# Performance work log

Hardware: AMD Instinct MI355X
Metric: run time of the kernel (lower is better)

Reference implementation:

```python
import jax, jax.numpy as jnp
import numpy as np

N = 100000      # nodes
E = 1600000     # edges
G = 64          # graphs in batch
H = 128         # hidden (== num_features)
L = 4           # num_layers
C = 16          # num_classes
NCAND = 100000  # candidate edges
BN_EPS = 1e-5


def setup_inputs() -> dict:
    key = jax.random.key(0)
    ks = jax.random.split(key, 24)
    s = 0.05
    inp = {}
    inp["x"] = jax.random.normal(ks[0], (N, H), dtype=jnp.float32)
    inp["edge_index"] = jax.random.randint(ks[1], (2, E), 0, N)
    inp["batch"] = jnp.sort(jax.random.randint(ks[2], (N,), 0, G))
    inp["candidate_edges"] = jax.random.randint(ks[3], (2, NCAND), 0, N)
    # GIN conv params, stacked over L layers (all layers are H->H since num_features==hidden)
    inp["cW1"] = jax.random.normal(ks[4], (L, H, H), dtype=jnp.float32) * s
    inp["cb1"] = jnp.zeros((L, H), jnp.float32)
    inp["cW2"] = jax.random.normal(ks[5], (L, H, H), dtype=jnp.float32) * s
    inp["cb2"] = jnp.zeros((L, H), jnp.float32)
    inp["cgamma"] = jnp.ones((L, H), jnp.float32)
    inp["cbeta"] = jnp.zeros((L, H), jnp.float32)
    inp["ceps"] = jnp.zeros((L,), jnp.float32)  # train_eps=True, init 0
    # node classifier: L*H -> 2H -> H -> H -> C (dropout is identity in eval)
    inp["ncW1"] = jax.random.normal(ks[6], (L * H, 2 * H), dtype=jnp.float32) * s
    inp["ncb1"] = jnp.zeros((2 * H,), jnp.float32)
    inp["ncW2"] = jax.random.normal(ks[7], (2 * H, H), dtype=jnp.float32) * s
    inp["ncb2"] = jnp.zeros((H,), jnp.float32)
    inp["ncW3"] = jax.random.normal(ks[8], (H, H), dtype=jnp.float32) * s
    inp["ncb3"] = jnp.zeros((H,), jnp.float32)
    inp["ncW4"] = jax.random.normal(ks[9], (H, C), dtype=jnp.float32) * s
    inp["ncb4"] = jnp.zeros((C,), jnp.float32)
    # edge predictor: 2*L*H -> 2H -> H -> 1
    inp["epW1"] = jax.random.normal(ks[10], (2 * L * H, 2 * H), dtype=jnp.float32) * s
    inp["epb1"] = jnp.zeros((2 * H,), jnp.float32)
    inp["epW2"] = jax.random.normal(ks[11], (2 * H, H), dtype=jnp.float32) * s
    inp["epb2"] = jnp.zeros((H,), jnp.float32)
    inp["epW3"] = jax.random.normal(ks[12], (H, 1), dtype=jnp.float32) * s
    inp["epb3"] = jnp.zeros((1,), jnp.float32)
    return inp


def _forward(x, cW1, cb1, cW2, cb2, cgamma, cbeta, ceps,
             ncW1, ncb1, ncW2, ncb2, ncW3, ncb3, ncW4, ncb4,
             epW1, epb1, epW2, epb2, epW3, epb3,
             edge_index, batch, candidate_edges):
    src, dst = edge_index[0], edge_index[1]
    h = x
    xs = []
    for l in range(L):
        # GIN: (1+eps)*x_i + sum_{j->i} x_j  (scatter-add over destination nodes)
        agg = jax.ops.segment_sum(h[src], dst, num_segments=N)
        z = (1.0 + ceps[l]) * h + agg
        z = jax.nn.relu(z @ cW1[l] + cb1[l])
        z = jax.nn.relu(z @ cW2[l] + cb2[l])
        # BatchNorm1d (training-mode batch statistics, biased variance)
        mu = z.mean(axis=0)
        var = jnp.var(z, axis=0)
        h = (z - mu) * jax.lax.rsqrt(var + BN_EPS) * cgamma[l] + cbeta[l]
        xs.append(h)
    emb = jnp.concatenate(xs, axis=-1)  # [N, L*H]
    # global mean pool over graphs
    sums = jax.ops.segment_sum(emb, batch, num_segments=G)
    cnt = jax.ops.segment_sum(jnp.ones((N, 1), emb.dtype), batch, num_segments=G)
    gemb = sums / jnp.maximum(cnt, 1.0)  # [G, L*H]
    t = jax.nn.relu(gemb @ ncW1 + ncb1)
    t = jax.nn.relu(t @ ncW2 + ncb2)
    t = jax.nn.relu(t @ ncW3 + ncb3)
    class_output = jax.nn.log_softmax(t @ ncW4 + ncb4, axis=1)  # [G, C]
    # link prediction: gather node embeddings per candidate edge
    ef = jnp.concatenate([emb[candidate_edges[0]], emb[candidate_edges[1]]], axis=1)  # [NC, 2*L*H]
    u = jax.nn.relu(ef @ epW1 + epb1)
    u = jax.nn.relu(u @ epW2 + epb2)
    edge_scores = jax.nn.sigmoid((u @ epW3 + epb3).squeeze(-1))  # [NC]
    return class_output, edge_scores


def reference(x, cW1, cb1, cW2, cb2, cgamma, cbeta, ceps,
              ncW1, ncb1, ncW2, ncb2, ncW3, ncb3, ncW4, ncb4,
              epW1, epb1, epW2, epb2, epW3, epb3,
              edge_index, batch, candidate_edges):
    return _forward(x, cW1, cb1, cW2, cb2, cgamma, cbeta, ceps,
                    ncW1, ncb1, ncW2, ncb2, ncW3, ncb3, ncW4, ncb4,
                    epW1, epb1, epW2, epb2, epW3, epb3,
                    edge_index, batch, candidate_edges)
```

## Files before the change

kernel.cpp:

```cpp
#include <hip/hip_runtime.h>
#include <math.h>

#define NN 100000
#define EE 1600000
#define GG 64
#define HH 128
#define LL 4
#define CCLS 16
#define NC 100000
#define NB 49
#define LDK 40
#define LDA2 136

typedef __attribute__((ext_vector_type(8))) short bf16x8;
typedef __attribute__((ext_vector_type(4))) float f32x4;

__device__ __forceinline__ unsigned short f2bf(float x) {
  union { float f; unsigned int u; } v; v.f = x;
  unsigned int r = v.u + 0x7fffu + ((v.u >> 16) & 1u);
  return (unsigned short)(r >> 16);
}
__device__ __forceinline__ float bl(unsigned u) {
  union { unsigned u; float f; } v; v.u = u << 16; return v.f;
}
__device__ __forceinline__ float bh(unsigned u) {
  union { unsigned u; float f; } v; v.u = u & 0xffff0000u; return v.f;
}

__global__ void hist_kernel(const int* __restrict__ dst, int* __restrict__ cnt, int E) {
  int e = blockIdx.x * 256 + threadIdx.x;
  if (e < E) atomicAdd(&cnt[dst[e]], 1);
}

__global__ __launch_bounds__(256) void scan_p1(const int* __restrict__ cnt,
                                               int* __restrict__ bsum, int n) {
  __shared__ int red[256];
  int tid = threadIdx.x;
  int base = blockIdx.x * 1024 + tid * 4;
  int s = 0;
  if (base + 3 < n) {
    int4 v = *(const int4*)(cnt + base);
    s = v.x + v.y + v.z + v.w;
  } else {
    for (int i = 0; i < 4; ++i) if (base + i < n) s += cnt[base + i];
  }
  red[tid] = s;
  __syncthreads();
  for (int st = 128; st >= 1; st >>= 1) {
    if (tid < st) red[tid] += red[tid + st];
    __syncthreads();
  }
  if (tid == 0) bsum[blockIdx.x] = red[0];
}

__global__ void scan_p2(int* __restrict__ bsum, int* __restrict__ rowptr,
                        int* __restrict__ bcursor, int nb, int n) {
  __shared__ int buf[128];
  int tid = threadIdx.x;
  int v = (tid < nb) ? bsum[tid] : 0;
  buf[tid] = v;
  __syncthreads();
  for (int off = 1; off < 128; off <<= 1) {
    int t = (tid >= off) ? buf[tid - off] : 0;
    __syncthreads();
    buf[tid] += t;
    __syncthreads();
  }
  if (tid < nb) bsum[tid] = buf[tid] - v;
  if (tid == 127) rowptr[n] = buf[127];
  __syncthreads();
  if (tid < NB) bcursor[tid] = bsum[2 * tid];
}

__global__ __launch_bounds__(256) void scan_p3(const int* __restrict__ cnt,
                                               const int* __restrict__ bsum,
                                               int* __restrict__ rowptr,
                                               int* __restrict__ cursor, int n) {
  __shared__ int red[256];
  int tid = threadIdx.x;
  int base = blockIdx.x * 1024 + tid * 4;
  int v[4] = {0, 0, 0, 0};
  if (base + 3 < n) {
    int4 t = *(const int4*)(cnt + base);
    v[0] = t.x; v[1] = t.y; v[2] = t.z; v[3] = t.w;
  } else {
    for (int i = 0; i < 4; ++i) if (base + i < n) v[i] = cnt[base + i];
  }
  int s = v[0] + v[1] + v[2] + v[3];
  red[tid] = s;
  __syncthreads();
  for (int off = 1; off < 256; off <<= 1) {
    int t = (tid >= off) ? red[tid - off] : 0;
    __syncthreads();
    red[tid] += t;
    __syncthreads();
  }
  int run = bsum[blockIdx.x] + red[tid] - s;
  int4 o;
  o.x = run; o.y = run + v[0]; o.z = o.y + v[1]; o.w = o.z + v[2];
  if (base + 3 < n) {
    *(int4*)(rowptr + base) = o;
    *(int4*)(cursor + base) = o;
  } else {
    int oo[4] = {o.x, o.y, o.z, o.w};
    for (int i = 0; i < 4; ++i)
      if (base + i < n) { rowptr[base + i] = oo[i]; cursor[base + i] = oo[i]; }
  }
}

__global__ __launch_bounds__(256) void partition_kernel(const int* __restrict__ src,
                                                        const int* __restrict__ dst,
                                                        int* __restrict__ bcursor,
                                                        int2* __restrict__ pairs, int E) {
  __shared__ int sS[4096];
  __shared__ int sD[4096];
  __shared__ int hist[NB];
  __shared__ int base[NB];
  int tid = threadIdx.x;
  int base_e = blockIdx.x * 4096;
  int cnt = min(4096, E - base_e);
  if (tid < NB) hist[tid] = 0;
  for (int i = tid * 4; i < cnt; i += 1024) {
    if (i + 3 < cnt) {
      *(int4*)(sS + i) = *(const int4*)(src + base_e + i);
      *(int4*)(sD + i) = *(const int4*)(dst + base_e + i);
    } else {
      for (int k = i; k < cnt; ++k) { sS[k] = src[base_e + k]; sD[k] = dst[base_e + k]; }
    }
  }
  __syncthreads();
  for (int i = tid; i < cnt; i += 256) atomicAdd(&hist[sD[i] >> 11], 1);
  __syncthreads();
  if (tid < NB) {
    base[tid] = atomicAdd(&bcursor[tid], hist[tid]);
    hist[tid] = 0;
  }
  __syncthreads();
  for (int i = tid; i < cnt; i += 256) {
    int d = sD[i];
    int b = d >> 11;
    int off = atomicAdd(&hist[b], 1);
    pairs[base[b] + off] = make_int2(sS[i], d);
  }
}

__global__ __launch_bounds__(256) void scatter_csr(const int2* __restrict__ pairs,
                                                   const int* __restrict__ rowptr,
                                                   int* __restrict__ cursor,
                                                   int* __restrict__ csr_src) {
  int b = blockIdx.x % 56;
  int slice = blockIdx.x / 56;
  if (b >= NB) return;
  int start = rowptr[b * 2048];
  int endn = min((b + 1) * 2048, NN);
  int end = rowptr[endn];
  for (int i = start + slice * 256 + threadIdx.x; i < end; i += 8 * 256) {
    int2 p = pairs[i];
    int pos = atomicAdd(&cursor[p.y], 1);
    csr_src[pos] = p.x;
  }
}

__global__ void f2b4_kernel(const float* __restrict__ in, unsigned short* __restrict__ out, int n4) {
  int i = blockIdx.x * 256 + threadIdx.x;
  if (i >= n4) return;
  float4 v = ((const float4*)in)[i];
  unsigned short r[4] = {f2bf(v.x), f2bf(v.y), f2bf(v.z), f2bf(v.w)};
  *(uint2*)(out + (size_t)i * 4) = *(uint2*)r;
}

__global__ void conv_weights(const float* __restrict__ cW1, const float* __restrict__ cW2,
                             unsigned short* __restrict__ WT1, unsigned short* __restrict__ WT2,
                             const float* __restrict__ epW1, unsigned short* __restrict__ W1T,
                             const float* __restrict__ epW2, unsigned short* __restrict__ W2T) {
  int idx = blockIdx.x * 256 + threadIdx.x;
  if (idx < LL * 16384) {
    int l = idx >> 14, r = idx & 16383, k = r >> 7, n = r & 127;
    WT1[l * 16384 + n * 128 + k] = f2bf(cW1[idx]);
    WT2[l * 16384 + n * 128 + k] = f2bf(cW2[idx]);
  } else if (idx < LL * 16384 + 262144) {
    int j = idx - LL * 16384;
    int k = j >> 8, n = j & 255;
    W1T[(size_t)n * 1024 + k] = f2bf(epW1[j]);
  } else if (idx < LL * 16384 + 262144 + 32768) {
    int j = idx - LL * 16384 - 262144;
    int k = j >> 7, n = j & 127;
    W2T[(size_t)n * 256 + k] = f2bf(epW2[j]);
  }
}

__global__ void aggregate_bf16(const unsigned short* __restrict__ h16, int ld,
                               const int* __restrict__ rowptr,
                               const int* __restrict__ csr_src,
                               const float* __restrict__ ceps_l,
                               unsigned short* __restrict__ out, int n) {
  int wave = threadIdx.x >> 6;
  int lane = threadIdx.x & 63;
  int sub = lane >> 4;
  int li = lane & 15;
  int node = blockIdx.x * 16 + wave * 4 + sub;
  if (node >= n) return;
  int c8 = li * 8;
  float eps1 = 1.0f + *ceps_l;
  float acc[8] = {};
  int b = rowptr[node], e = rowptr[node + 1];
  int j = b;
  for (; j + 8 <= e; j += 8) {
    uint4 u[8];
#pragma unroll
    for (int t = 0; t < 8; ++t) {
      int s = csr_src[j + t];
      u[t] = *(const uint4*)(h16 + (size_t)s * ld + c8);
    }
#pragma unroll
    for (int t = 0; t < 8; ++t) {
      acc[0] += bl(u[t].x); acc[1] += bh(u[t].x);
      acc[2] += bl(u[t].y); acc[3] += bh(u[t].y);
      acc[4] += bl(u[t].z); acc[5] += bh(u[t].z);
      acc[6] += bl(u[t].w); acc[7] += bh(u[t].w);
    }
  }
  for (; j < e; ++j) {
    int s = csr_src[j];
    uint4 u = *(const uint4*)(h16 + (size_t)s * ld + c8);
    acc[0] += bl(u.x); acc[1] += bh(u.x);
    acc[2] += bl(u.y); acc[3] += bh(u.y);
    acc[4] += bl(u.z); acc[5] += bh(u.z);
    acc[6] += bl(u.w); acc[7] += bh(u.w);
  }
  uint4 hu = *(const uint4*)(h16 + (size_t)node * ld + c8);
  acc[0] = fmaf(eps1, bl(hu.x), acc[0]); acc[1] = fmaf(eps1, bh(hu.x), acc[1]);
  acc[2] = fmaf(eps1, bl(hu.y), acc[2]); acc[3] = fmaf(eps1, bh(hu.y), acc[3]);
  acc[4] = fmaf(eps1, bl(hu.z), acc[4]); acc[5] = fmaf(eps1, bh(hu.z), acc[5]);
  acc[6] = fmaf(eps1, bl(hu.w), acc[6]); acc[7] = fmaf(eps1, bh(hu.w), acc[7]);
  unsigned short o[8];
#pragma unroll
  for (int i = 0; i < 8; ++i) o[i] = f2bf(acc[i]);
  *(uint4*)(out + (size_t)node * 128 + c8) = *(uint4*)o;
}

__global__ __launch_bounds__(256) void trunk_fused(
    const unsigned short* __restrict__ A16,
    const unsigned short* __restrict__ W1T, const float* __restrict__ b1,
    const unsigned short* __restrict__ W2T, const float* __restrict__ b2,
    float* __restrict__ bnsum, float* __restrict__ bnsumsq,
    unsigned short* __restrict__ C16, int M) {
  __shared__ unsigned short As[128 * LDA2];
  __shared__ unsigned short Bs[128 * LDK];
  const int tid = threadIdx.x;
  const int bm = blockIdx.x * 128;
  const int lane = tid & 63;
  const int wave = tid >> 6;
  const int wr = (wave >> 1) << 6;
  const int wc = (wave & 1) << 6;
  const int ar = tid >> 1;
  const int ah = (tid & 1) << 4;
  int gra = bm + ar; if (gra >= M) gra = M - 1;
  const unsigned short* Arow = A16 + (size_t)gra * 128;
  const int mrow = lane & 15;
  const int kq = (lane >> 4) << 3;
  f32x4 acc[4][4] = {};

#pragma unroll
  for (int ks = 0; ks < 4; ++ks) {
    const int k0 = ks << 5;
    const uint4* s = (const uint4*)(Arow + k0 + ah);
    *(uint4*)(As + ar * LDA2 + k0 + ah) = s[0];
    *(uint4*)(As + ar * LDA2 + k0 + ah + 8) = s[1];
  }
  uint4 p0 = *(const uint4*)(W1T + (size_t)ar * 128 + ah);
  uint4 p1 = *(const uint4*)(W1T + (size_t)ar * 128 + ah + 8);
  for (int ks = 0; ks < 4; ++ks) {
    const int k0 = ks << 5;
    *(uint4*)(Bs + ar * LDK + ah) = p0;
    *(uint4*)(Bs + ar * LDK + ah + 8) = p1;
    __syncthreads();
    if (ks < 3) {
      p0 = *(const uint4*)(W1T + (size_t)ar * 128 + k0 + 32 + ah);
      p1 = *(const uint4*)(W1T + (size_t)ar * 128 + k0 + 32 + ah + 8);
    }
    bf16x8 af[4], bfv[4];
#pragma unroll
    for (int t = 0; t < 4; ++t)
      af[t] = *(const bf16x8*)(As + (wr + t * 16 + mrow) * LDA2 + k0 + kq);
#pragma unroll
    for (int t = 0; t < 4; ++t)
      bfv[t] = *(const bf16x8*)(Bs + (wc + t * 16 + mrow) * LDK + kq);
#pragma unroll
    for (int mt = 0; mt < 4; ++mt)
#pragma unroll
      for (int nt = 0; nt < 4; ++nt)
        acc[mt][nt] = __builtin_amdgcn_mfma_f32_16x16x32_bf16(af[mt], bfv[nt], acc[mt][nt], 0, 0, 0);
    __syncthreads();
  }
  const int crow = (lane >> 4) << 2;
  const int ccol = lane & 15;
#pragma unroll
  for (int nt = 0; nt < 4; ++nt) {
    int c = wc + nt * 16 + ccol;
    float bz = b1[c];
#pragma unroll
    for (int mt = 0; mt < 4; ++mt) {
      int rl = wr + mt * 16 + crow;
#pragma unroll
      for (int i = 0; i < 4; ++i)
        As[(rl + i) * LDA2 + c] = f2bf(fmaxf(acc[mt][nt][i] + bz, 0.f));
    }
  }
#pragma unroll
  for (int mt = 0; mt < 4; ++mt)
#pragma unroll
    for (int nt = 0; nt < 4; ++nt)
      acc[mt][nt] = (f32x4){0.f, 0.f, 0.f, 0.f};
  p0 = *(const uint4*)(W2T + (size_t)ar * 128 + ah);
  p1 = *(const uint4*)(W2T + (size_t)ar * 128 + ah + 8);
  __syncthreads();
  for (int ks = 0; ks < 4; ++ks) {
    const int k0 = ks << 5;
    *(uint4*)(Bs + ar * LDK + ah) = p0;
    *(uint4*)(Bs + ar * LDK + ah + 8) = p1;
    __syncthreads();
    if (ks < 3) {
      p0 = *(const uint4*)(W2T + (size_t)ar * 128 + k0 + 32 + ah);
      p1 = *(const uint4*)(W2T + (size_t)ar * 128 + k0 + 32 + ah + 8);
    }
    bf16x8 af[4], bfv[4];
#pragma unroll
    for (int t = 0; t < 4; ++t)
      af[t] = *(const bf16x8*)(As + (wr + t * 16 + mrow) * LDA2 + k0 + kq);
#pragma unroll
    for (int t = 0; t < 4; ++t)
      bfv[t] = *(const bf16x8*)(Bs + (wc + t * 16 + mrow) * LDK + kq);
#pragma unroll
    for (int mt = 0; mt < 4; ++mt)
#pragma unroll
      for (int nt = 0; nt < 4; ++nt)
        acc[mt][nt] = __builtin_amdgcn_mfma_f32_16x16x32_bf16(af[mt], bfv[nt], acc[mt][nt], 0, 0, 0);
    __syncthreads();
  }
#pragma unroll
  for (int nt = 0; nt < 4; ++nt) {
    int c = wc + nt * 16 + ccol;
    float bz = b2[c];
    float s = 0.f, q = 0.f;
#pragma unroll
    for (int mt = 0; mt < 4; ++mt) {
      int rbase = bm + wr + mt * 16 + crow;
#pragma unroll
      for (int i = 0; i < 4; ++i) {
        int r = rbase + i;
        if (r < M) {
          float v = fmaxf(acc[mt][nt][i] + bz, 0.f);
          C16[(size_t)r * 128 + c] = f2bf(v);
          s += v; q += v * v;
        }
      }
    }
    s += __shfl_xor(s, 16, 64);
    s += __shfl_xor(s, 32, 64);
    q += __shfl_xor(q, 16, 64);
    q += __shfl_xor(q, 32, 64);
    if (lane < 16) {
      atomicAdd(&bnsum[c], s);
      atomicAdd(&bnsumsq[c], q);
    }
  }
}

__global__ __launch_bounds__(512) void mfma_gemm_gather(
    const unsigned short* __restrict__ emb16, const int* __restrict__ cand,
    const unsigned short* __restrict__ WT ,
    const float* __restrict__ bias,
    unsigned short* __restrict__ C16 , int M) {
  __shared__ unsigned short As[2][128 * LDK];
  __shared__ unsigned short Bs[2][256 * LDK];
  const int tid = threadIdx.x;
  const int bm = blockIdx.x * 128;
  const int lane = tid & 63;
  const int wave = tid >> 6;
  const int wr = (wave >> 2) << 6;
  const int wc = (wave & 3) << 6;
  f32x4 acc[4][4] = {};
  const int ar = tid >> 2;
  const int ah = (tid & 3) << 3;
  int gra = bm + ar; if (gra >= M) gra = M - 1;
  const int node0 = cand[gra];
  const int node1 = cand[NC + gra];
  const int br = tid >> 1;
  const int bh8 = (tid & 1) << 4;
  const unsigned short* Brow = WT + (size_t)br * 1024 + bh8;
  const int mrow = lane & 15;
  const int kq = (lane >> 4) << 3;

  {
    uint4 a = *(const uint4*)(emb16 + (size_t)node0 * 512 + ah);
    uint4 b0 = *(const uint4*)(Brow);
    uint4 b1 = *(const uint4*)(Brow + 8);
    *(uint4*)(As[0] + ar * LDK + ah) = a;
    *(uint4*)(Bs[0] + br * LDK + bh8) = b0;
    *(uint4*)(Bs[0] + br * LDK + bh8 + 8) = b1;
  }
  __syncthreads();
  for (int ks = 0; ks < 32; ++ks) {
    const int cur = ks & 1, nxt = cur ^ 1;
    uint4 a, b0, b1;
    if (ks < 31) {
      const int k1 = (ks + 1) << 5;
      int node = (k1 < 512) ? node0 : node1;
      a = *(const uint4*)(emb16 + (size_t)node * 512 + (k1 & 511) + ah);
      b0 = *(const uint4*)(Brow + k1);
      b1 = *(const uint4*)(Brow + k1 + 8);
    }
    bf16x8 af[4], bfv[4];
#pragma unroll
    for (int t = 0; t < 4; ++t)
      af[t] = *(const bf16x8*)(As[cur] + (wr + t * 16 + mrow) * LDK + kq);
#pragma unroll
    for (int t = 0; t < 4; ++t)
      bfv[t] = *(const bf16x8*)(Bs[cur] + (wc + t * 16 + mrow) * LDK + kq);
#pragma unroll
    for (int mt = 0; mt < 4; ++mt)
#pragma unroll
      for (int nt = 0; nt < 4; ++nt)
        acc[mt][nt] = __builtin_amdgcn_mfma_f32_16x16x32_bf16(af[mt], bfv[nt], acc[mt][nt], 0, 0, 0);
    if (ks < 31) {
      *(uint4*)(As[nxt] + ar * LDK + ah) = a;
      *(uint4*)(Bs[nxt] + br * LDK + bh8) = b0;
      *(uint4*)(Bs[nxt] + br * LDK + bh8 + 8) = b1;
      __syncthreads();
    }
  }
  const int crow = (lane >> 4) << 2;
  const int ccol = lane & 15;
#pragma unroll
  for (int nt = 0; nt < 4; ++nt) {
    int cbase = wc + nt * 16 + ccol;
    float bz = bias[cbase];
#pragma unroll
    for (int mt = 0; mt < 4; ++mt) {
      int rbase = bm + wr + mt * 16 + crow;
#pragma unroll
      for (int i = 0; i < 4; ++i) {
        int r = rbase + i;
        if (r < M) C16[(size_t)r * 256 + cbase] = f2bf(fmaxf(acc[mt][nt][i] + bz, 0.f));
      }
    }
  }
}

__global__ __launch_bounds__(256) void ep_gemm2_final(
    const unsigned short* __restrict__ A16 ,
    const unsigned short* __restrict__ WT ,
    const float* __restrict__ b2, const float* __restrict__ epW3,
    const float* __restrict__ epb3,
    float* __restrict__ out, int M) {
  __shared__ unsigned short As[2][128 * LDK];
  __shared__ unsigned short Bs[2][128 * LDK];
  __shared__ float sDot[128];
  const int tid = threadIdx.x;
  const int bm = blockIdx.x * 128;
  const int lane = tid & 63;
  const int wave = tid >> 6;
  const int wr = (wave >> 1) << 6;
  const int wc = (wave & 1) << 6;
  f32x4 acc[4][4] = {};
  const int ar = tid >> 1;
  const int ah = (tid & 1) << 4;
  int gra = bm + ar; if (gra >= M) gra = M - 1;
  const unsigned short* Arow = A16 + (size_t)gra * 256;
  const unsigned short* Brow = WT + (size_t)ar * 256;
  const int mrow = lane & 15;
  const int kq = (lane >> 4) << 3;

  if (tid < 128) sDot[tid] = 0.f;
  {
    uint4 a0 = *(const uint4*)(Arow + ah);
    uint4 a1 = *(const uint4*)(Arow + ah + 8);
    uint4 b0 = *(const uint4*)(Brow + ah);
    uint4 b1 = *(const uint4*)(Brow + ah + 8);
    *(uint4*)(As[0] + ar * LDK + ah) = a0;
    *(uint4*)(As[0] + ar * LDK + ah + 8) = a1;
    *(uint4*)(Bs[0] + ar * LDK + ah) = b0;
    *(uint4*)(Bs[0] + ar * LDK + ah + 8) = b1;
  }
  __syncthreads();
  for (int ks = 0; ks < 8; ++ks) {
    const int cur = ks & 1, nxt = cur ^ 1;
    uint4 a0, a1, b0, b1;
    if (ks < 7) {
      const int k1 = (ks + 1) << 5;
      a0 = *(const uint4*)(Arow + k1 + ah);
      a1 = *(const uint4*)(Arow + k1 + ah + 8);
      b0 = *(const uint4*)(Brow + k1 + ah);
      b1 = *(const uint4*)(Brow + k1 + ah + 8);
    }
    bf16x8 af[4], bfv[4];
#pragma unroll
    for (int t = 0; t < 4; ++t)
      af[t] = *(const bf16x8*)(As[cur] + (wr + t * 16 + mrow) * LDK + kq);
#pragma unroll
    for (int t = 0; t < 4; ++t)
      bfv[t] = *(const bf16x8*)(Bs[cur] + (wc + t * 16 + mrow) * LDK + kq);
#pragma unroll
    for (int mt = 0; mt < 4; ++mt)
#pragma unroll
      for (int nt = 0; nt < 4; ++nt)
        acc[mt][nt] = __builtin_amdgcn_mfma_f32_16x16x32_bf16(af[mt], bfv[nt], acc[mt][nt], 0, 0, 0);
    if (ks < 7) {
      *(uint4*)(As[nxt] + ar * LDK + ah) = a0;
      *(uint4*)(As[nxt] + ar * LDK + ah + 8) = a1;
      *(uint4*)(Bs[nxt] + ar * LDK + ah) = b0;
      *(uint4*)(Bs[nxt] + ar * LDK + ah + 8) = b1;
      __syncthreads();
    }
  }
  const int crow = (lane >> 4) << 2;
  const int ccol = lane & 15;
  float w3v[4], bz[4];
#pragma unroll
  for (int nt = 0; nt < 4; ++nt) {
    int c = wc + nt * 16 + ccol;
    w3v[nt] = epW3[c];
    bz[nt] = b2[c];
  }
  __syncthreads();
#pragma unroll
  for (int mt = 0; mt < 4; ++mt) {
#pragma unroll
    for (int i = 0; i < 4; ++i) {
      int rl = wr + mt * 16 + crow + i;
      float p = 0.f;
#pragma unroll
      for (int nt = 0; nt < 4; ++nt)
        p = fmaf(fmaxf(acc[mt][nt][i] + bz[nt], 0.f), w3v[nt], p);
      atomicAdd(&sDot[rl], p);
    }
  }
  __syncthreads();
  if (tid < 128) {
    int r = bm + tid;
    if (r < M) out[r] = 1.f / (1.f + expf(-(sDot[tid] + epb3[0])));
  }
}

__global__ void bn_apply_bf16(const unsigned short* __restrict__ z,
                              const float* __restrict__ sum, const float* __restrict__ sumsq,
                              const float* __restrict__ gamma, const float* __restrict__ beta,
                              unsigned short* __restrict__ out, int n) {
  int idx = blockIdx.x * 256 + threadIdx.x;
  if (idx >= n * 16) return;
  int r = idx >> 4, c8 = (idx & 15) << 3;
  uint4 v = *(const uint4*)(z + (size_t)r * 128 + c8);
  float f[8] = {bl(v.x), bh(v.x), bl(v.y), bh(v.y), bl(v.z), bh(v.z), bl(v.w), bh(v.w)};
  const float inv_n = 1.0f / (float)NN;
  unsigned short o[8];
#pragma unroll
  for (int j = 0; j < 8; ++j) {
    int c = c8 + j;
    float mu = sum[c] * inv_n;
    float var = sumsq[c] * inv_n - mu * mu;
    float sc = rsqrtf(var + 1e-5f) * gamma[c];
    o[j] = f2bf((f[j] - mu) * sc + beta[c]);
  }
  *(uint4*)(out + (size_t)r * 512 + c8) = *(uint4*)o;
}

__global__ void bounds_kernel(const int* __restrict__ batch, int* __restrict__ gstart, int n) {
  int g = threadIdx.x;
  if (g > GG) return;
  int lo = 0, hi = n;
  while (lo < hi) {
    int mid = (lo + hi) >> 1;
    if (batch[mid] < g) lo = mid + 1; else hi = mid;
  }
  gstart[g] = lo;
}

__global__ __launch_bounds__(256) void pool_bf16(const unsigned short* __restrict__ emb16,
                                                 const int* __restrict__ gstart,
                                                 float* __restrict__ gsum) {
  int g = blockIdx.x;
  int chunk = blockIdx.y;
  int c2 = threadIdx.x * 2;
  int s = gstart[g], e = gstart[g + 1];
  int len = e - s;
  int per = (len + 7) >> 3;
  int r0 = s + chunk * per;
  int r1 = min(r0 + per, e);
  float ax = 0.f, ay = 0.f;
  for (int r = r0; r < r1; ++r) {
    unsigned u = *(const unsigned*)(emb16 + (size_t)r * 512 + c2);
    ax += bl(u); ay += bh(u);
  }
  if (r1 > r0) {
    atomicAdd(&gsum[g * 512 + c2], ax);
    atomicAdd(&gsum[g * 512 + c2 + 1], ay);
  }
}

__global__ __launch_bounds__(256) void nc_fused(
    const float* __restrict__ gsum, const int* __restrict__ gstart,
    const float* __restrict__ W1, const float* __restrict__ b1,
    const float* __restrict__ W2, const float* __restrict__ b2,
    const float* __restrict__ W3, const float* __restrict__ b3,
    const float* __restrict__ W4, const float* __restrict__ b4,
    float* __restrict__ out) {
  __shared__ float row[512];
  __shared__ float t1[256];
  __shared__ float t2[128];
  __shared__ float t3s[128];
  __shared__ float lg[16];
  int g = blockIdx.x;
  int tid = threadIdx.x;
  float inv = 1.0f / fmaxf((float)(gstart[g + 1] - gstart[g]), 1.0f);
  row[tid] = gsum[g * 512 + tid] * inv;
  row[tid + 256] = gsum[g * 512 + tid + 256] * inv;
  __syncthreads();
  {
    float acc = b1[tid];
#pragma unroll 8
    for (int k = 0; k < 512; ++k) acc = fmaf(row[k], W1[k * 256 + tid], acc);
    t1[tid] = fmaxf(acc, 0.f);
  }
  __syncthreads();
  if (tid < 128) {
    float acc = b2[tid];
#pragma unroll 8
    for (int k = 0; k < 256; ++k) acc = fmaf(t1[k], W2[k * 128 + tid], acc);
    t2[tid] = fmaxf(acc, 0.f);
  }
  __syncthreads();
  if (tid < 128) {
    float acc = b3[tid];
#pragma unroll 8
    for (int k = 0; k < 128; ++k) acc = fmaf(t2[k], W3[k * 128 + tid], acc);
    t3s[tid] = fmaxf(acc, 0.f);
  }
  __syncthreads();
  if (tid < 16) {
    float acc = b4[tid];
#pragma unroll 8
    for (int k = 0; k < 128; ++k) acc = fmaf(t3s[k], W4[k * 16 + tid], acc);
    lg[tid] = acc;
  }
  __syncthreads();
  if (tid < 16) {
    float v = lg[tid];
    float m = v;
    for (int j = 0; j < 16; ++j) m = fmaxf(m, lg[j]);
    float s = 0.f;
    for (int j = 0; j < 16; ++j) s += expf(lg[j] - m);
    out[g * 16 + tid] = v - m - logf(s);
  }
}

extern "C" void kernel_launch(void* const* d_in, const int* in_sizes, int n_in,
                              void* d_out, int out_size, void* d_ws, size_t ws_size,
                              hipStream_t stream) {
  const float* x = (const float*)d_in[0];
  const int* edge_index = (const int*)d_in[1];
  const int* batch = (const int*)d_in[2];
  const int* cand = (const int*)d_in[3];
  const float* cW1 = (const float*)d_in[4];
  const float* cb1 = (const float*)d_in[5];
  const float* cW2 = (const float*)d_in[6];
  const float* cb2 = (const float*)d_in[7];
  const float* cgamma = (const float*)d_in[8];
  const float* cbeta = (const float*)d_in[9];
  const float* ceps = (const float*)d_in[10];
  const float* ncW1 = (const float*)d_in[11];
  const float* ncb1 = (const float*)d_in[12];
  const float* ncW2 = (const float*)d_in[13];
  const float* ncb2 = (const float*)d_in[14];
  const float* ncW3 = (const float*)d_in[15];
  const float* ncb3 = (const float*)d_in[16];
  const float* ncW4 = (const float*)d_in[17];
  const float* ncb4 = (const float*)d_in[18];
  const float* epW1 = (const float*)d_in[19];
  const float* epb1 = (const float*)d_in[20];
  const float* epW2 = (const float*)d_in[21];
  const float* epb2 = (const float*)d_in[22];
  const float* epW3 = (const float*)d_in[23];
  const float* epb3 = (const float*)d_in[24];

  char* ws = (char*)d_ws;
  size_t off = 0;
  auto alloc = [&](size_t bytes) -> void* {
    off = (off + 255) & ~(size_t)255;
    void* p = ws + off;
    off += bytes;
    return p;
  };
  size_t zz_bytes = (size_t)NN * 4 + 512 * 4 + 512 * 4 + (size_t)GG * 512 * 4;
  char* zz = (char*)alloc(zz_bytes);
  int* cnt = (int*)zz;
  float* bnsum = (float*)(zz + (size_t)NN * 4);
  float* bnsumsq = bnsum + 512;
  float* gsum = bnsumsq + 512;
  int* rowptr = (int*)alloc((size_t)(NN + 1) * 4);
  int* cursor = (int*)alloc((size_t)NN * 4);
  int* csr_src = (int*)alloc((size_t)EE * 4);
  int2* pairs = (int2*)alloc((size_t)EE * 8);
  int* bsum = (int*)alloc(128 * 4);
  int* bcursor = (int*)alloc(64 * 4);
  unsigned short* x16 = (unsigned short*)alloc((size_t)NN * 128 * 2);
  unsigned short* g16a = (unsigned short*)alloc((size_t)NN * 128 * 2);
  unsigned short* emb16 = (unsigned short*)alloc((size_t)NN * 512 * 2);
  unsigned short* C1 = (unsigned short*)alloc((size_t)NC * 256 * 2);
  unsigned short* WT1 = (unsigned short*)alloc((size_t)LL * 16384 * 2);
  unsigned short* WT2 = (unsigned short*)alloc((size_t)LL * 16384 * 2);
  unsigned short* W1T = (unsigned short*)alloc((size_t)1024 * 256 * 2);
  unsigned short* W2T = (unsigned short*)alloc((size_t)256 * 128 * 2);
  int* gstart = (int*)alloc(65 * 4);

  const int* esrc = edge_index;
  const int* edst = edge_index + EE;
  const int nblk = (NN + 1023) / 1024;
  const int nech = (EE + 4095) / 4096;

  hipMemsetAsync(zz, 0, zz_bytes, stream);
  hist_kernel<<<(EE + 255) / 256, 256, 0, stream>>>(edst, cnt, EE);
  scan_p1<<<nblk, 256, 0, stream>>>(cnt, bsum, NN);
  scan_p2<<<1, 128, 0, stream>>>(bsum, rowptr, bcursor, nblk, NN);
  scan_p3<<<nblk, 256, 0, stream>>>(cnt, bsum, rowptr, cursor, NN);
  partition_kernel<<<nech, 256, 0, stream>>>(esrc, edst, bcursor, pairs, EE);
  scatter_csr<<<56 * 8, 256, 0, stream>>>(pairs, rowptr, cursor, csr_src);
  f2b4_kernel<<<(NN * 128 / 4 + 255) / 256, 256, 0, stream>>>(x, x16, NN * 128 / 4);
  conv_weights<<<(LL * 16384 + 262144 + 32768 + 255) / 256, 256, 0, stream>>>(
      cW1, cW2, WT1, WT2, epW1, W1T, epW2, W2T);

  for (int l = 0; l < LL; ++l) {
    const unsigned short* h16 = (l == 0) ? x16 : (emb16 + (size_t)(l - 1) * 128);
    int ld = (l == 0) ? 128 : 512;
    aggregate_bf16<<<(NN + 15) / 16, 256, 0, stream>>>(h16, ld, rowptr, csr_src, ceps + l, g16a, NN);
    trunk_fused<<<(NN + 127) / 128, 256, 0, stream>>>(
        g16a, WT1 + (size_t)l * 16384, cb1 + l * 128,
        WT2 + (size_t)l * 16384, cb2 + l * 128,
        bnsum + l * 128, bnsumsq + l * 128, g16a, NN);
    bn_apply_bf16<<<(NN * 16 + 255) / 256, 256, 0, stream>>>(
        g16a, bnsum + l * 128, bnsumsq + l * 128, cgamma + l * 128, cbeta + l * 128,
        emb16 + (size_t)l * 128, NN);
  }

  bounds_kernel<<<1, 128, 0, stream>>>(batch, gstart, NN);
  pool_bf16<<<dim3(GG, 8), 256, 0, stream>>>(emb16, gstart, gsum);
  nc_fused<<<GG, 256, 0, stream>>>(gsum, gstart, ncW1, ncb1, ncW2, ncb2, ncW3, ncb3,
                                   ncW4, ncb4, (float*)d_out);

  mfma_gemm_gather<<<(NC + 127) / 128, 512, 0, stream>>>(emb16, cand, W1T, epb1, C1, NC);
  ep_gemm2_final<<<(NC + 127) / 128, 256, 0, stream>>>(C1, W2T, epb2, epW3, epb3,
                                                       (float*)d_out + GG * CCLS, NC);
}
```

Before: 1.120 ms.

## Fuse aggregation into layer GEMM and fold BatchNorm into downstream consumers

The separate per-layer aggregation and BN-apply kernels are removed. Each layer kernel now gathers neighbour rows straight into shared memory, applies the previous layer's BN affine analytically (scaling the sum and adding degree times the shift), then runs the MLP and writes raw post-ReLU activations into the embedding buffer. The final BN affine is folded into the edge-predictor first-layer weights and bias and into the pooled graph embeddings. This removes several full-size bf16 round trips and launches per layer. The cost is gather work serialized within each GEMM block, which may hurt latency hiding, and some extra rounding from the folded weights.

New measurement: 1.231 ms. 9.9% more time.

```diff
diff --git a/kernel.cpp b/kernel.cpp
--- a/kernel.cpp
+++ b/kernel.cpp
@@ -171,80 +171,59 @@
 
 __global__ void conv_weights(const float* __restrict__ cW1, const float* __restrict__ cW2,
                              unsigned short* __restrict__ WT1, unsigned short* __restrict__ WT2,
-                             const float* __restrict__ epW1, unsigned short* __restrict__ W1T,
                              const float* __restrict__ epW2, unsigned short* __restrict__ W2T) {
   int idx = blockIdx.x * 256 + threadIdx.x;
   if (idx < LL * 16384) {
     int l = idx >> 14, r = idx & 16383, k = r >> 7, n = r & 127;
     WT1[l * 16384 + n * 128 + k] = f2bf(cW1[idx]);
     WT2[l * 16384 + n * 128 + k] = f2bf(cW2[idx]);
-  } else if (idx < LL * 16384 + 262144) {
+  } else if (idx < LL * 16384 + 32768) {
     int j = idx - LL * 16384;
-    int k = j >> 8, n = j & 255;
-    W1T[(size_t)n * 1024 + k] = f2bf(epW1[j]);
-  } else if (idx < LL * 16384 + 262144 + 32768) {
-    int j = idx - LL * 16384 - 262144;
     int k = j >> 7, n = j & 127;
     W2T[(size_t)n * 256 + k] = f2bf(epW2[j]);
   }
 }
 
-__global__ void aggregate_bf16(const unsigned short* __restrict__ h16, int ld,
-                               const int* __restrict__ rowptr,
-                               const int* __restrict__ csr_src,
-                               const float* __restrict__ ceps_l,
-                               unsigned short* __restrict__ out, int n) {
-  int wave = threadIdx.x >> 6;
-  int lane = threadIdx.x & 63;
-  int sub = lane >> 4;
-  int li = lane & 15;
-  int node = blockIdx.x * 16 + wave * 4 + sub;
-  if (node >= n) return;
-  int c8 = li * 8;
-  float eps1 = 1.0f + *ceps_l;
-  float acc[8] = {};
-  int b = rowptr[node], e = rowptr[node + 1];
-  int j = b;
-  for (; j + 8 <= e; j += 8) {
-    uint4 u[8];
-#pragma unroll
-    for (int t = 0; t < 8; ++t) {
-      int s = csr_src[j + t];
-      u[t] = *(const uint4*)(h16 + (size_t)s * ld + c8);
-    }
-#pragma unroll
-    for (int t = 0; t < 8; ++t) {
-      acc[0] += bl(u[t].x); acc[1] += bh(u[t].x);
-      acc[2] += bl(u[t].y); acc[3] += bh(u[t].y);
-      acc[4] += bl(u[t].z); acc[5] += bh(u[t].z);
-      acc[6] += bl(u[t].w); acc[7] += bh(u[t].w);
-    }
-  }
-  for (; j < e; ++j) {
-    int s = csr_src[j];
-    uint4 u = *(const uint4*)(h16 + (size_t)s * ld + c8);
-    acc[0] += bl(u.x); acc[1] += bh(u.x);
-    acc[2] += bl(u.y); acc[3] += bh(u.y);
-    acc[4] += bl(u.z); acc[5] += bh(u.z);
-    acc[6] += bl(u.w); acc[7] += bh(u.w);
-  }
-  uint4 hu = *(const uint4*)(h16 + (size_t)node * ld + c8);
-  acc[0] = fmaf(eps1, bl(hu.x), acc[0]); acc[1] = fmaf(eps1, bh(hu.x), acc[1]);
-  acc[2] = fmaf(eps1, bl(hu.y), acc[2]); acc[3] = fmaf(eps1, bh(hu.y), acc[3]);
-  acc[4] = fmaf(eps1, bl(hu.z), acc[4]); acc[5] = fmaf(eps1, bh(hu.z), acc[5]);
-  acc[6] = fmaf(eps1, bl(hu.w), acc[6]); acc[7] = fmaf(eps1, bh(hu.w), acc[7]);
-  unsigned short o[8];
-#pragma unroll
-  for (int i = 0; i < 8; ++i) o[i] = f2bf(acc[i]);
-  *(uint4*)(out + (size_t)node * 128 + c8) = *(uint4*)o;
-}
-
-__global__ __launch_bounds__(256) void trunk_fused(
-    const unsigned short* __restrict__ A16,
+__global__ void bn_coef(const float* __restrict__ bnsum, const float* __restrict__ bnsumsq,
+                        const float* __restrict__ cgamma, const float* __restrict__ cbeta,
+                        float* __restrict__ abuf, float* __restrict__ bbuf) {
+  int c = blockIdx.x * 256 + threadIdx.x;
+  if (c >= 512) return;
+  const float inv_n = 1.0f / (float)NN;
+  float mu = bnsum[c] * inv_n;
+  float var = bnsumsq[c] * inv_n - mu * mu;
+  float sc = rsqrtf(var + 1e-5f) * cgamma[c];
+  abuf[c] = sc;
+  bbuf[c] = cbeta[c] - mu * sc;
+}
+
+__global__ void fold_w1(const float* __restrict__ epW1, const float* __restrict__ abuf,
+                        unsigned short* __restrict__ W1Tf) {
+  int idx = blockIdx.x * 256 + threadIdx.x;
+  if (idx >= 262144) return;
+  int k = idx >> 8, n = idx & 255;
+  W1Tf[(size_t)n * 1024 + k] = f2bf(epW1[idx] * abuf[k & 511]);
+}
+
+__global__ void fold_b1(const float* __restrict__ epW1, const float* __restrict__ bbuf,
+                        const float* __restrict__ epb1, float* __restrict__ epb1f) {
+  int n = threadIdx.x;
+  float acc = epb1[n];
+#pragma unroll 8
+  for (int k = 0; k < 1024; ++k) acc = fmaf(bbuf[k & 511], epW1[k * 256 + n], acc);
+  epb1f[n] = acc;
+}
+
+__global__ __launch_bounds__(256) void layer_fused(
+    const unsigned short* __restrict__ h_raw, int ld, int has_bn,
+    const float* __restrict__ psum, const float* __restrict__ psq,
+    const float* __restrict__ pgamma, const float* __restrict__ pbeta,
+    const float* __restrict__ ceps_l,
+    const int* __restrict__ rowptr, const int* __restrict__ csr_src,
     const unsigned short* __restrict__ W1T, const float* __restrict__ b1,
     const unsigned short* __restrict__ W2T, const float* __restrict__ b2,
     float* __restrict__ bnsum, float* __restrict__ bnsumsq,
-    unsigned short* __restrict__ C16, int M) {
+    unsigned short* __restrict__ zout, int M) {
   __shared__ unsigned short As[128 * LDA2];
   __shared__ unsigned short Bs[128 * LDK];
   const int tid = threadIdx.x;
@@ -255,21 +234,77 @@
   const int wc = (wave & 1) << 6;
   const int ar = tid >> 1;
   const int ah = (tid & 1) << 4;
-  int gra = bm + ar; if (gra >= M) gra = M - 1;
-  const unsigned short* Arow = A16 + (size_t)gra * 128;
   const int mrow = lane & 15;
   const int kq = (lane >> 4) << 3;
-  f32x4 acc[4][4] = {};
-
-#pragma unroll
-  for (int ks = 0; ks < 4; ++ks) {
-    const int k0 = ks << 5;
-    const uint4* s = (const uint4*)(Arow + k0 + ah);
-    *(uint4*)(As + ar * LDA2 + k0 + ah) = s[0];
-    *(uint4*)(As + ar * LDA2 + k0 + ah + 8) = s[1];
-  }
+
   uint4 p0 = *(const uint4*)(W1T + (size_t)ar * 128 + ah);
   uint4 p1 = *(const uint4*)(W1T + (size_t)ar * 128 + ah + 8);
+
+  {
+    int sub = tid >> 4;
+    int li = tid & 15;
+    int c8 = li * 8;
+    float a[8], bc[8];
+    if (has_bn) {
+      const float inv_n = 1.0f / (float)NN;
+#pragma unroll
+      for (int j = 0; j < 8; ++j) {
+        int c = c8 + j;
+        float mu = psum[c] * inv_n;
+        float var = psq[c] * inv_n - mu * mu;
+        float sc = rsqrtf(var + 1e-5f) * pgamma[c];
+        a[j] = sc;
+        bc[j] = pbeta[c] - mu * sc;
+      }
+    } else {
+#pragma unroll
+      for (int j = 0; j < 8; ++j) { a[j] = 1.f; bc[j] = 0.f; }
+    }
+    float eps1 = 1.0f + *ceps_l;
+    for (int t = 0; t < 8; ++t) {
+      int node = bm + sub * 8 + t;
+      int nn = (node < M) ? node : (M - 1);
+      float acc[8] = {};
+      int bgn = rowptr[nn], end = rowptr[nn + 1];
+      int j = bgn;
+      for (; j + 8 <= end; j += 8) {
+        uint4 u[8];
+#pragma unroll
+        for (int q = 0; q < 8; ++q) {
+          int s = csr_src[j + q];
+          u[q] = *(const uint4*)(h_raw + (size_t)s * ld + c8);
+        }
+#pragma unroll
+        for (int q = 0; q < 8; ++q) {
+          acc[0] += bl(u[q].x); acc[1] += bh(u[q].x);
+          acc[2] += bl(u[q].y); acc[3] += bh(u[q].y);
+          acc[4] += bl(u[q].z); acc[5] += bh(u[q].z);
+          acc[6] += bl(u[q].w); acc[7] += bh(u[q].w);
+        }
+      }
+      for (; j < end; ++j) {
+        int s = csr_src[j];
+        uint4 u = *(const uint4*)(h_raw + (size_t)s * ld + c8);
+        acc[0] += bl(u.x); acc[1] += bh(u.x);
+        acc[2] += bl(u.y); acc[3] += bh(u.y);
+        acc[4] += bl(u.z); acc[5] += bh(u.z);
+        acc[6] += bl(u.w); acc[7] += bh(u.w);
+      }
+      uint4 hu = *(const uint4*)(h_raw + (size_t)nn * ld + c8);
+      acc[0] = fmaf(eps1, bl(hu.x), acc[0]); acc[1] = fmaf(eps1, bh(hu.x), acc[1]);
+      acc[2] = fmaf(eps1, bl(hu.y), acc[2]); acc[3] = fmaf(eps1, bh(hu.y), acc[3]);
+      acc[4] = fmaf(eps1, bl(hu.z), acc[4]); acc[5] = fmaf(eps1, bh(hu.z), acc[5]);
+      acc[6] = fmaf(eps1, bl(hu.w), acc[6]); acc[7] = fmaf(eps1, bh(hu.w), acc[7]);
+      float degb = (float)(end - bgn) + eps1;
+      unsigned short o[8];
+#pragma unroll
+      for (int i2 = 0; i2 < 8; ++i2) o[i2] = f2bf(fmaf(a[i2], acc[i2], degb * bc[i2]));
+      *(uint4*)(As + (sub * 8 + t) * LDA2 + c8) = *(uint4*)o;
+    }
+  }
+  __syncthreads();
+
+  f32x4 acc[4][4] = {};
   for (int ks = 0; ks < 4; ++ks) {
     const int k0 = ks << 5;
     *(uint4*)(Bs + ar * LDK + ah) = p0;
@@ -351,7 +386,7 @@
         int r = rbase + i;
         if (r < M) {
           float v = fmaxf(acc[mt][nt][i] + bz, 0.f);
-          C16[(size_t)r * 128 + c] = f2bf(v);
+          zout[(size_t)r * 512 + c] = f2bf(v);
           s += v; q += v * v;
         }
       }
@@ -543,28 +578,6 @@
   }
 }
 
-__global__ void bn_apply_bf16(const unsigned short* __restrict__ z,
-                              const float* __restrict__ sum, const float* __restrict__ sumsq,
-                              const float* __restrict__ gamma, const float* __restrict__ beta,
-                              unsigned short* __restrict__ out, int n) {
-  int idx = blockIdx.x * 256 + threadIdx.x;
-  if (idx >= n * 16) return;
-  int r = idx >> 4, c8 = (idx & 15) << 3;
-  uint4 v = *(const uint4*)(z + (size_t)r * 128 + c8);
-  float f[8] = {bl(v.x), bh(v.x), bl(v.y), bh(v.y), bl(v.z), bh(v.z), bl(v.w), bh(v.w)};
-  const float inv_n = 1.0f / (float)NN;
-  unsigned short o[8];
-#pragma unroll
-  for (int j = 0; j < 8; ++j) {
-    int c = c8 + j;
-    float mu = sum[c] * inv_n;
-    float var = sumsq[c] * inv_n - mu * mu;
-    float sc = rsqrtf(var + 1e-5f) * gamma[c];
-    o[j] = f2bf((f[j] - mu) * sc + beta[c]);
-  }
-  *(uint4*)(out + (size_t)r * 512 + c8) = *(uint4*)o;
-}
-
 __global__ void bounds_kernel(const int* __restrict__ batch, int* __restrict__ gstart, int n) {
   int g = threadIdx.x;
   if (g > GG) return;
@@ -598,8 +611,20 @@
   }
 }
 
+__global__ void pool_div(const float* __restrict__ gsum, const int* __restrict__ gstart,
+                         const float* __restrict__ abuf, const float* __restrict__ bbuf,
+                         float* __restrict__ gemb) {
+  int idx = blockIdx.x * 256 + threadIdx.x;
+  if (idx >= GG * 512) return;
+  int g = idx >> 9, c = idx & 511;
+  int s = gstart[g], e = gstart[g + 1];
+  float len = (float)(e - s);
+  float cntf = fmaxf(len, 1.0f);
+  gemb[idx] = (abuf[c] * gsum[idx] + len * bbuf[c]) / cntf;
+}
+
 __global__ __launch_bounds__(256) void nc_fused(
-    const float* __restrict__ gsum, const int* __restrict__ gstart,
+    const float* __restrict__ gemb,
     const float* __restrict__ W1, const float* __restrict__ b1,
     const float* __restrict__ W2, const float* __restrict__ b2,
     const float* __restrict__ W3, const float* __restrict__ b3,
@@ -612,9 +637,8 @@
   __shared__ float lg[16];
   int g = blockIdx.x;
   int tid = threadIdx.x;
-  float inv = 1.0f / fmaxf((float)(gstart[g + 1] - gstart[g]), 1.0f);
-  row[tid] = gsum[g * 512 + tid] * inv;
-  row[tid + 256] = gsum[g * 512 + tid + 256] * inv;
+  row[tid] = gemb[g * 512 + tid];
+  row[tid + 256] = gemb[g * 512 + tid + 256];
   __syncthreads();
   {
     float acc = b1[tid];
@@ -704,13 +728,16 @@
   int* bsum = (int*)alloc(128 * 4);
   int* bcursor = (int*)alloc(64 * 4);
   unsigned short* x16 = (unsigned short*)alloc((size_t)NN * 128 * 2);
-  unsigned short* g16a = (unsigned short*)alloc((size_t)NN * 128 * 2);
   unsigned short* emb16 = (unsigned short*)alloc((size_t)NN * 512 * 2);
   unsigned short* C1 = (unsigned short*)alloc((size_t)NC * 256 * 2);
   unsigned short* WT1 = (unsigned short*)alloc((size_t)LL * 16384 * 2);
   unsigned short* WT2 = (unsigned short*)alloc((size_t)LL * 16384 * 2);
-  unsigned short* W1T = (unsigned short*)alloc((size_t)1024 * 256 * 2);
+  unsigned short* W1Tf = (unsigned short*)alloc((size_t)1024 * 256 * 2);
   unsigned short* W2T = (unsigned short*)alloc((size_t)256 * 128 * 2);
+  float* abuf = (float*)alloc(512 * 4);
+  float* bbuf = (float*)alloc(512 * 4);
+  float* epb1f = (float*)alloc(256 * 4);
+  float* gemb = (float*)alloc((size_t)GG * 512 * 4);
   int* gstart = (int*)alloc(65 * 4);
 
   const int* esrc = edge_index;
@@ -726,28 +753,34 @@
   partition_kernel<<<nech, 256, 0, stream>>>(esrc, edst, bcursor, pairs, EE);
   scatter_csr<<<56 * 8, 256, 0, stream>>>(pairs, rowptr, cursor, csr_src);
   f2b4_kernel<<<(NN * 128 / 4 + 255) / 256, 256, 0, stream>>>(x, x16, NN * 128 / 4);
-  conv_weights<<<(LL * 16384 + 262144 + 32768 + 255) / 256, 256, 0, stream>>>(
-      cW1, cW2, WT1, WT2, epW1, W1T, epW2, W2T);
+  conv_weights<<<(LL * 16384 + 32768 + 255) / 256, 256, 0, stream>>>(
+      cW1, cW2, WT1, WT2, epW2, W2T);
 
   for (int l = 0; l < LL; ++l) {
-    const unsigned short* h16 = (l == 0) ? x16 : (emb16 + (size_t)(l - 1) * 128);
+    const unsigned short* h = (l == 0) ? x16 : (emb16 + (size_t)(l - 1) * 128);
     int ld = (l == 0) ? 128 : 512;
-    aggregate_bf16<<<(NN + 15) / 16, 256, 0, stream>>>(h16, ld, rowptr, csr_src, ceps + l, g16a, NN);
-    trunk_fused<<<(NN + 127) / 128, 256, 0, stream>>>(
-        g16a, WT1 + (size_t)l * 16384, cb1 + l * 128,
+    layer_fused<<<(NN + 127) / 128, 256, 0, stream>>>(
+        h, ld, (l > 0) ? 1 : 0,
+        bnsum + (l - 1) * 128, bnsumsq + (l - 1) * 128,
+        cgamma + (l - 1) * 128, cbeta + (l - 1) * 128,
+        ceps + l, rowptr, csr_src,
+        WT1 + (size_t)l * 16384, cb1 + l * 128,
         WT2 + (size_t)l * 16384, cb2 + l * 128,
-        bnsum + l * 128, bnsumsq + l * 128, g16a, NN);
-    bn_apply_bf16<<<(NN * 16 + 255) / 256, 256, 0, stream>>>(
-        g16a, bnsum + l * 128, bnsumsq + l * 128, cgamma + l * 128, cbeta + l * 128,
+        bnsum + l * 128, bnsumsq + l * 128,
         emb16 + (size_t)l * 128, NN);
   }
+
+  bn_coef<<<2, 256, 0, stream>>>(bnsum, bnsumsq, cgamma, cbeta, abuf, bbuf);
+  fold_w1<<<(262144 + 255) / 256, 256, 0, stream>>>(epW1, abuf, W1Tf);
+  fold_b1<<<1, 256, 0, stream>>>(epW1, bbuf, epb1, epb1f);
 
   bounds_kernel<<<1, 128, 0, stream>>>(batch, gstart, NN);
   pool_bf16<<<dim3(GG, 8), 256, 0, stream>>>(emb16, gstart, gsum);
-  nc_fused<<<GG, 256, 0, stream>>>(gsum, gstart, ncW1, ncb1, ncW2, ncb2, ncW3, ncb3,
+  pool_div<<<(GG * 512 + 255) / 256, 256, 0, stream>>>(gsum, gstart, abuf, bbuf, gemb);
+  nc_fused<<<GG, 256, 0, stream>>>(gemb, ncW1, ncb1, ncW2, ncb2, ncW3, ncb3,
                                    ncW4, ncb4, (float*)d_out);
 
-  mfma_gemm_gather<<<(NC + 127) / 128, 512, 0, stream>>>(emb16, cand, W1T, epb1, C1, NC);
+  mfma_gemm_gather<<<(NC + 127) / 128, 512, 0, stream>>>(emb16, cand, W1Tf, epb1f, C1, NC);
   ep_gemm2_final<<<(NC + 127) / 128, 256, 0, stream>>>(C1, W2T, epb2, epW3, epb3,
                                                        (float*)d_out + GG * CCLS, NC);
 }
```
